# Performance work log

Hardware: AMD Instinct MI355X
Metric: run time of the kernel (lower is better)

The kernel has to match this reference:

```python
import jax, jax.numpy as jnp
import numpy as np

N_EMBD = 256
N_HEAD = 8
BATCH = 4
SEQ = 2048
NEG_BIAS = -1000000000.0


def setup_inputs() -> dict:
    key = jax.random.key(0)
    ks = jax.random.split(key, 5)
    scale = 1.0 / np.sqrt(N_EMBD)
    x = jax.random.normal(ks[0], (BATCH, SEQ, N_EMBD), dtype=jnp.float32)
    # torch Linear weight layout: (out_features, in_features)
    Wq = jax.random.normal(ks[1], (N_EMBD * N_HEAD, N_EMBD), dtype=jnp.float32) * scale
    Wk = jax.random.normal(ks[2], (N_EMBD * N_HEAD, N_EMBD), dtype=jnp.float32) * scale
    Wv = jax.random.normal(ks[3], (N_EMBD * N_HEAD, N_EMBD), dtype=jnp.float32) * scale
    Wo = jax.random.normal(ks[4], (N_EMBD, N_EMBD * N_HEAD), dtype=jnp.float32) * scale / np.sqrt(N_HEAD)
    return {"x": x, "Wq": Wq, "Wk": Wk, "Wv": Wv, "Wo": Wo}


def reference(x, Wq, Wk, Wv, Wo):
    B, L, E = x.shape
    H, D = N_HEAD, N_EMBD  # d_head == n_embd in this module
    # projections: x @ W.T, then split heads -> (B, H, L, D)
    def proj(W):
        y = jnp.einsum('ble,fe->blf', x, W)  # (B, L, H*D)
        return y.reshape(B, L, H, D).transpose(0, 2, 1, 3)
    q, k, v = proj(Wq), proj(Wk), proj(Wv)
    scores = jnp.einsum('bhld,bhmd->bhlm', q, k) * (E ** -0.5)
    # first (non-causal) softmax over full rows
    attn = jax.nn.softmax(scores, axis=-1)
    # causal mask replaces disallowed probs with large negative bias, then softmax again
    causal = jnp.tril(jnp.ones((L, L), dtype=bool))
    attn = jnp.where(causal[None, None], attn, jnp.asarray(NEG_BIAS, attn.dtype))
    attn = jax.nn.softmax(attn, axis=-1)
    out = jnp.einsum('bhlm,bhmd->bhld', attn, v)  # (B, H, L, D)
    out = out.transpose(0, 2, 1, 3).reshape(B, L, H * D)
    return jnp.einsum('blf,ef->ble', out, Wo)  # (B, L, E)
```

## Files before the change

kernel.cpp:

```cpp
#include <hip/hip_runtime.h>
#include <stdint.h>

typedef unsigned short ushort_t;
typedef __attribute__((ext_vector_type(8))) short bf16x8;
typedef __attribute__((ext_vector_type(4))) short s16x4;
typedef __attribute__((ext_vector_type(4))) float f32x4;
typedef __attribute__((ext_vector_type(4))) unsigned short us4;

#define DEV __device__ __forceinline__

DEV ushort_t f2bf(float f) {
    unsigned int u = __float_as_uint(f);
    u += 0x7fffu + ((u >> 16) & 1u);
    return (ushort_t)(u >> 16);
}

DEV void async16(const ushort_t* g, ushort_t* l) {
    __builtin_amdgcn_global_load_lds(
        (const __attribute__((address_space(1))) void*)g,
        (__attribute__((address_space(3))) void*)l,
        16, 0, 0);
}

DEV void barrier_lgkm() {
    __asm__ volatile("s_waitcnt lgkmcnt(0)\n\ts_barrier" ::: "memory");
}
DEV void barrier_vm8() {
    __asm__ volatile("s_waitcnt vmcnt(8)\n\ts_barrier" ::: "memory");
}
DEV void barrier_vm0() {
    __asm__ volatile("s_waitcnt vmcnt(0)\n\ts_barrier" ::: "memory");
}

__global__ void convert_kernel(const float* __restrict__ x, const float* __restrict__ wq,
                               const float* __restrict__ wk, const float* __restrict__ wv,
                               const float* __restrict__ wo,
                               ushort_t* __restrict__ xb, ushort_t* __restrict__ wqb,
                               ushort_t* __restrict__ wkb, ushort_t* __restrict__ wvb,
                               ushort_t* __restrict__ wob)
{
    const int i = blockIdx.x * 256 + threadIdx.x;
    const float* src; ushort_t* dst; int off;
    if (i < 524288)      { src = x;  dst = xb;  off = i; }
    else if (i < 655360) { src = wq; dst = wqb; off = i - 524288; }
    else if (i < 786432) { src = wk; dst = wkb; off = i - 655360; }
    else if (i < 917504) { src = wv; dst = wvb; off = i - 786432; }
    else                 { src = wo; dst = wob; off = i - 917504; }
    const float4 v = ((const float4*)src)[off];
    us4 o;
    o[0] = f2bf(v.x); o[1] = f2bf(v.y); o[2] = f2bf(v.z); o[3] = f2bf(v.w);
    ((us4*)dst)[off] = o;
}

__global__ __launch_bounds__(256, 2) void gemm_qkv_kernel(
    const ushort_t* __restrict__ A, const ushort_t* __restrict__ Bm,
    void* __restrict__ C0, void* __restrict__ C1, void* __restrict__ C2)
{
    __shared__ ushort_t At[128 * 64];
    __shared__ ushort_t Bt[128 * 64];

    const int tid  = threadIdx.x;
    const int wave = tid >> 6;
    const int lane = tid & 63;
    const int quad = lane >> 4;
    const int l15  = lane & 15;
    const int mhalf = wave >> 1;
    const int nhalf = wave & 1;
    const int m0 = blockIdx.x * 128;
    const int n0 = blockIdx.y * 128;
    const int K = 256;

    f32x4 acc[4][4];
#pragma unroll
    for (int mf = 0; mf < 4; ++mf)
#pragma unroll
        for (int nf = 0; nf < 4; ++nf)
#pragma unroll
            for (int r = 0; r < 4; ++r) acc[mf][nf][r] = 0.f;

    const int crow = (lane & 7) ^ (lane >> 3);

    for (int k0 = 0; k0 < K; k0 += 64) {
        __syncthreads();
#pragma unroll
        for (int t = 0; t < 4; ++t) {
            const int row = wave * 32 + t * 8 + (lane >> 3);
            async16(A + (size_t)(m0 + row) * K + k0 + crow * 8,
                    At + (wave * 32 + t * 8) * 64 + lane * 8);
            async16(Bm + (size_t)(n0 + row) * K + k0 + crow * 8,
                    Bt + (wave * 32 + t * 8) * 64 + lane * 8);
        }
        __syncthreads();
#pragma unroll
        for (int ks = 0; ks < 2; ++ks) {
            bf16x8 af[4], bf[4];
#pragma unroll
            for (int mf = 0; mf < 4; ++mf) {
                const int ml = mhalf * 64 + mf * 16 + l15;
                const int c = (ks * 4 + quad) ^ (ml & 7);
                af[mf] = *(const bf16x8*)(At + ml * 64 + c * 8);
            }
#pragma unroll
            for (int nf = 0; nf < 4; ++nf) {
                const int nl = nhalf * 64 + nf * 16 + l15;
                const int c = (ks * 4 + quad) ^ (nl & 7);
                bf[nf] = *(const bf16x8*)(Bt + nl * 64 + c * 8);
            }
#pragma unroll
            for (int mf = 0; mf < 4; ++mf)
#pragma unroll
                for (int nf = 0; nf < 4; ++nf)
                    acc[mf][nf] = __builtin_amdgcn_mfma_f32_16x16x32_bf16(
                        af[mf], bf[nf], acc[mf][nf], 0, 0, 0);
        }
    }

    const int sel = n0 >> 11;
    if (sel == 2) {
#pragma unroll
        for (int mf = 0; mf < 4; ++mf)
#pragma unroll
            for (int nf = 0; nf < 4; ++nf) {
                const int row = m0 + mhalf * 64 + mf * 16 + quad * 4;
                const int colv = (n0 - 4096) + nhalf * 64 + nf * 16 + l15;
                const int b_ = row >> 11, l_ = row & 2047;
                const int h_ = colv >> 8, d_ = colv & 255;
                us4 pk;
#pragma unroll
                for (int r = 0; r < 4; ++r) pk[r] = f2bf(acc[mf][nf][r]);
                *(us4*)((ushort_t*)C2 +
                        (((size_t)(b_ * 8 + h_) * 256 + d_) * 2048 + l_)) = pk;
            }
    } else {
        ushort_t* dst = sel ? (ushort_t*)C1 : (ushort_t*)C0;
#pragma unroll
        for (int mf = 0; mf < 4; ++mf)
#pragma unroll
            for (int nf = 0; nf < 4; ++nf)
#pragma unroll
                for (int r = 0; r < 4; ++r) {
                    const int row = m0 + mhalf * 64 + mf * 16 + quad * 4 + r;
                    const int col = (n0 & 2047) + nhalf * 64 + nf * 16 + l15;
                    dst[(size_t)row * 2048 + col] = f2bf(acc[mf][nf][r]);
                }
    }
}

__global__ __launch_bounds__(256, 4) void gemm_out_kernel(
    const ushort_t* __restrict__ A, const ushort_t* __restrict__ Bm,
    float* __restrict__ C)
{
    __shared__ ushort_t At[64 * 64];
    __shared__ ushort_t Bt[128 * 64];

    const int tid  = threadIdx.x;
    const int wave = tid >> 6;
    const int lane = tid & 63;
    const int quad = lane >> 4;
    const int l15  = lane & 15;
    const int mhalf = wave >> 1;
    const int nhalf = wave & 1;
    const int m0 = blockIdx.x * 64;
    const int n0 = blockIdx.y * 128;

    f32x4 acc[2][4];
#pragma unroll
    for (int mf = 0; mf < 2; ++mf)
#pragma unroll
        for (int nf = 0; nf < 4; ++nf)
#pragma unroll
            for (int r = 0; r < 4; ++r) acc[mf][nf][r] = 0.f;

    const int crow = (lane & 7) ^ (lane >> 3);

    for (int k0 = 0; k0 < 2048; k0 += 64) {
        __syncthreads();
#pragma unroll
        for (int t = 0; t < 2; ++t) {
            const int row = wave * 16 + t * 8 + (lane >> 3);
            async16(A + (size_t)(m0 + row) * 2048 + k0 + crow * 8,
                    At + (wave * 16 + t * 8) * 64 + lane * 8);
        }
#pragma unroll
        for (int t = 0; t < 4; ++t) {
            const int row = wave * 32 + t * 8 + (lane >> 3);
            async16(Bm + (size_t)(n0 + row) * 2048 + k0 + crow * 8,
                    Bt + (wave * 32 + t * 8) * 64 + lane * 8);
        }
        __syncthreads();
#pragma unroll
        for (int ks = 0; ks < 2; ++ks) {
            bf16x8 af[2], bf[4];
#pragma unroll
            for (int mf = 0; mf < 2; ++mf) {
                const int ml = mhalf * 32 + mf * 16 + l15;
                const int c = (ks * 4 + quad) ^ (ml & 7);
                af[mf] = *(const bf16x8*)(At + ml * 64 + c * 8);
            }
#pragma unroll
            for (int nf = 0; nf < 4; ++nf) {
                const int nl = nhalf * 64 + nf * 16 + l15;
                const int c = (ks * 4 + quad) ^ (nl & 7);
                bf[nf] = *(const bf16x8*)(Bt + nl * 64 + c * 8);
            }
#pragma unroll
            for (int mf = 0; mf < 2; ++mf)
#pragma unroll
                for (int nf = 0; nf < 4; ++nf)
                    acc[mf][nf] = __builtin_amdgcn_mfma_f32_16x16x32_bf16(
                        af[mf], bf[nf], acc[mf][nf], 0, 0, 0);
        }
    }

#pragma unroll
    for (int mf = 0; mf < 2; ++mf)
#pragma unroll
        for (int nf = 0; nf < 4; ++nf)
#pragma unroll
            for (int r = 0; r < 4; ++r) {
                const int row = m0 + mhalf * 32 + mf * 16 + quad * 4 + r;
                const int col = n0 + nhalf * 64 + nf * 16 + l15;
                C[(size_t)row * 256 + col] = acc[mf][nf][r];
            }
}

__global__ __launch_bounds__(256, 4) void pass1_kernel(
    const ushort_t* __restrict__ q_ws, const ushort_t* __restrict__ k_ws,
    float* __restrict__ rz_ws)
{
    __shared__ ushort_t Kt[64 * 256];
    __shared__ float zred[2][64];

    const float SCALE = 0.0625f;
    const int tid  = threadIdx.x;
    const int wave = tid >> 6;
    const int lane = tid & 63;
    const int quad = lane >> 4;
    const int l15  = lane & 15;
    const int ihalf = wave >> 1;
    const int jhalf = wave & 1;

    const int g  = blockIdx.x;
    const int bh = ((g >> 8) << 3) | (g & 7);
    const int it = (g >> 3) & 31;
    const int b = bh >> 3, h = bh & 7;
    const int i0 = it * 64;

    const size_t qkbase = (size_t)b * 2048 * 2048 + (size_t)h * 256;

    bf16x8 qf[2][8];
#pragma unroll
    for (int ng = 0; ng < 2; ++ng) {
        const int i_l = ihalf * 32 + ng * 16 + l15;
        const ushort_t* qr = q_ws + qkbase + (size_t)(i0 + i_l) * 2048;
#pragma unroll
        for (int ks = 0; ks < 8; ++ks)
            qf[ng][ks] = *(const bf16x8*)(qr + ks * 32 + quad * 8);
    }

    float z[2] = {0.f, 0.f};

    for (int jt = 0; jt < 32; ++jt) {
        const int j0 = jt * 64;
        __syncthreads();
        {
            const ushort_t* kb = k_ws + qkbase + (size_t)j0 * 2048;
#pragma unroll
            for (int t = 0; t < 8; ++t) {
                const int row = wave * 16 + t * 2 + (lane >> 5);
                const int c = (lane & 31) ^ (row & 7);
                async16(kb + (size_t)row * 2048 + c * 8,
                        Kt + (wave * 16 + t * 2) * 256 + lane * 8);
            }
        }
        __syncthreads();

        f32x4 sacc[2][2];
#pragma unroll
        for (int a = 0; a < 2; ++a)
#pragma unroll
            for (int c = 0; c < 2; ++c)
#pragma unroll
                for (int r = 0; r < 4; ++r) sacc[a][c][r] = 0.f;

#pragma unroll
        for (int ks = 0; ks < 8; ++ks) {
            bf16x8 af[2];
#pragma unroll
            for (int mg = 0; mg < 2; ++mg) {
                const int j_l = jhalf * 32 + mg * 16 + l15;
                const int c = (ks * 4 + quad) ^ (j_l & 7);
                af[mg] = *(const bf16x8*)(Kt + j_l * 256 + c * 8);
            }
#pragma unroll
            for (int mg = 0; mg < 2; ++mg)
#pragma unroll
                for (int ng = 0; ng < 2; ++ng)
                    sacc[mg][ng] = __builtin_amdgcn_mfma_f32_16x16x32_bf16(
                        af[mg], qf[ng][ks], sacc[mg][ng], 0, 0, 0);
        }

#pragma unroll
        for (int ng = 0; ng < 2; ++ng)
#pragma unroll
            for (int mg = 0; mg < 2; ++mg)
#pragma unroll
                for (int r = 0; r < 4; ++r)
                    z[ng] += __expf(sacc[mg][ng][r] * SCALE);
    }

#pragma unroll
    for (int ng = 0; ng < 2; ++ng) {
        z[ng] += __shfl_xor(z[ng], 16);
        z[ng] += __shfl_xor(z[ng], 32);
    }
    __syncthreads();
    if (quad == 0) {
#pragma unroll
        for (int ng = 0; ng < 2; ++ng) {
            const int i_l = ihalf * 32 + ng * 16 + l15;
            zred[jhalf][i_l] = z[ng];
        }
    }
    __syncthreads();
    if (tid < 64)
        rz_ws[(size_t)bh * 2048 + i0 + tid] = 1.0f / (zred[0][tid] + zred[1][tid]);
}

__global__ __launch_bounds__(256, 1) void pass2_kernel(
    const ushort_t* __restrict__ q_ws, const ushort_t* __restrict__ k_ws,
    const ushort_t* __restrict__ vt_ws, const float* __restrict__ rz_ws,
    ushort_t* __restrict__ attn_out)
{
    __shared__ ushort_t Kb[2][32 * 256];
    __shared__ ushort_t Vb[2][256 * 32];
    __shared__ ushort_t Wt[64 * 32];
    __shared__ float dred[128];

    const float SCALE = 0.0625f;
    const int tid  = threadIdx.x;
    const int wave = tid >> 6;
    const int lane = tid & 63;
    const int quad = lane >> 4;
    const int l15  = lane & 15;
    const int ihalf = wave >> 1;
    const int jhalf = wave & 1;

    const int g  = blockIdx.x;
    const int bh = ((g >> 8) << 3) | (g & 7);
    const int it = 31 - ((g >> 3) & 31);
    const int b = bh >> 3, h = bh & 7;
    const int i0 = it * 64;
    const int jtmax = 2 * it + 1;

    const size_t qkbase = (size_t)b * 2048 * 2048 + (size_t)h * 256;
    const size_t vtbase = (size_t)bh * 256 * 2048;

    bf16x8 qf[2][8];
#pragma unroll
    for (int ng = 0; ng < 2; ++ng) {
        const int i_l = ihalf * 32 + ng * 16 + l15;
        const ushort_t* qr = q_ws + qkbase + (size_t)(i0 + i_l) * 2048;
#pragma unroll
        for (int ks = 0; ks < 8; ++ks)
            qf[ng][ks] = *(const bf16x8*)(qr + ks * 32 + quad * 8);
    }
    float rzrow[2];
#pragma unroll
    for (int ng = 0; ng < 2; ++ng)
        rzrow[ng] = rz_ws[(size_t)bh * 2048 + i0 + ihalf * 32 + ng * 16 + l15];

    f32x4 oacc[2][8];
#pragma unroll
    for (int mg = 0; mg < 2; ++mg)
#pragma unroll
        for (int nf = 0; nf < 8; ++nf)
#pragma unroll
            for (int r = 0; r < 4; ++r) oacc[mg][nf][r] = 0.f;
    float den[2] = {0.f, 0.f};

    const int krow_ = wave * 8 + (lane >> 5);
    const int vrow_ = wave * 64 + (lane >> 2);
#define STAGE_TILE(jt_, pb_)                                                  \
    {                                                                         \
        const ushort_t* kb_ = k_ws + qkbase + (size_t)(jt_) * 32 * 2048;      \
        const ushort_t* vb_ = vt_ws + vtbase + (size_t)(jt_) * 32;            \
        _Pragma("unroll")                                                     \
        for (int t = 0; t < 4; ++t) {                                         \
            const int kr = krow_ + t * 2;                                     \
            const int kc = (lane & 31) ^ (kr & 7);                            \
            async16(kb_ + (size_t)kr * 2048 + kc * 8,                         \
                    Kb[pb_] + (wave * 8 + t * 2) * 256 + lane * 8);           \
        }                                                                     \
        _Pragma("unroll")                                                     \
        for (int t = 0; t < 4; ++t) {                                         \
            const int vr = vrow_ + t * 16;                                    \
            const int vc = (lane & 3) ^ ((vr ^ (vr >> 2)) & 3);               \
            async16(vb_ + (size_t)vr * 2048 + vc * 8,                         \
                    Vb[pb_] + (wave * 64 + t * 16) * 32 + lane * 8);          \
        }                                                                     \
    }

    STAGE_TILE(0, 0);

    const int iblo = it * 4 + ihalf * 2;

    for (int jt = 0; jt <= jtmax; ++jt) {
        const int p = jt & 1;
        barrier_lgkm();
        if (jt < jtmax) {
            STAGE_TILE(jt + 1, 1 - p);
            barrier_vm8();
        } else {
            barrier_vm0();
        }

        const int jb16 = jt * 2 + jhalf;
        if (jb16 <= iblo + 1) {
            f32x4 sacc[2];
#pragma unroll
            for (int ng = 0; ng < 2; ++ng)
#pragma unroll
                for (int r = 0; r < 4; ++r) sacc[ng][r] = 0.f;
#pragma unroll
            for (int ks = 0; ks < 8; ++ks) {
                const int j_l = jhalf * 16 + l15;
                const int c = (ks * 4 + quad) ^ (j_l & 7);
                const bf16x8 af = *(const bf16x8*)(Kb[p] + j_l * 256 + c * 8);
#pragma unroll
                for (int ng = 0; ng < 2; ++ng)
                    sacc[ng] = __builtin_amdgcn_mfma_f32_16x16x32_bf16(
                        af, qf[ng][ks], sacc[ng], 0, 0, 0);
            }
            const bool need_mask = (jb16 >= iblo);
#pragma unroll
            for (int ng = 0; ng < 2; ++ng) {
                const int di = (i0 + ihalf * 32 + ng * 16 + l15)
                             - (jt * 32 + jhalf * 16 + quad * 4);
                us4 wp;
#pragma unroll
                for (int r = 0; r < 4; ++r) {
                    const float pr = __expf(sacc[ng][r] * SCALE) * rzrow[ng];
                    float w = __expf(pr);
                    if (need_mask && (r > di)) w = 0.f;
                    den[ng] += w;
                    wp[r] = f2bf(w);
                }
                const int row = ihalf * 32 + ng * 16 + l15;
                const int c = (jhalf * 4 + quad) ^ (l15 & 7);
                *(us4*)(Wt + row * 32 + c * 4) = wp;
            }
        } else {
            const us4 zz = {0, 0, 0, 0};
#pragma unroll
            for (int ng = 0; ng < 2; ++ng) {
                const int row = ihalf * 32 + ng * 16 + l15;
                const int c = (jhalf * 4 + quad) ^ (l15 & 7);
                *(us4*)(Wt + row * 32 + c * 4) = zz;
            }
        }
        barrier_lgkm();

        if (jt <= it * 2 + ihalf) {
            bf16x8 aw[2];
#pragma unroll
            for (int mg = 0; mg < 2; ++mg) {
                const int row = ihalf * 32 + mg * 16 + l15;
                const s16x4 lo = *(const s16x4*)(Wt + row * 32 + ((2 * quad)     ^ (l15 & 7)) * 4);
                const s16x4 hi = *(const s16x4*)(Wt + row * 32 + ((2 * quad + 1) ^ (l15 & 7)) * 4);
                union { s16x4 hh[2]; bf16x8 v; } u;
                u.hh[0] = lo; u.hh[1] = hi;
                aw[mg] = u.v;
            }
#pragma unroll
            for (int nf = 0; nf < 8; ++nf) {
                const int d = jhalf * 128 + nf * 16 + l15;
                const int c = quad ^ ((d ^ (d >> 2)) & 3);
                const bf16x8 bv = *(const bf16x8*)(Vb[p] + d * 32 + c * 8);
                oacc[0][nf] = __builtin_amdgcn_mfma_f32_16x16x32_bf16(aw[0], bv, oacc[0][nf], 0, 0, 0);
                oacc[1][nf] = __builtin_amdgcn_mfma_f32_16x16x32_bf16(aw[1], bv, oacc[1][nf], 0, 0, 0);
            }
        }
    }
#undef STAGE_TILE

#pragma unroll
    for (int ng = 0; ng < 2; ++ng) {
        den[ng] += __shfl_xor(den[ng], 16);
        den[ng] += __shfl_xor(den[ng], 32);
    }
    __syncthreads();
    if (quad == 0) {
#pragma unroll
        for (int ng = 0; ng < 2; ++ng)
            dred[(ihalf * 2 + jhalf) * 32 + ng * 16 + l15] = den[ng];
    }
    __syncthreads();
#pragma unroll
    for (int mg = 0; mg < 2; ++mg) {
#pragma unroll
        for (int r = 0; r < 4; ++r) {
            const int il = mg * 16 + quad * 4 + r;
            const float dt = dred[(ihalf * 2) * 32 + il] + dred[(ihalf * 2 + 1) * 32 + il];
            const float rd = 1.0f / dt;
            ushort_t* orow = attn_out + qkbase + (size_t)(i0 + ihalf * 32 + il) * 2048;
#pragma unroll
            for (int nf = 0; nf < 8; ++nf)
                orow[jhalf * 128 + nf * 16 + l15] = f2bf(oacc[mg][nf][r] * rd);
        }
    }
}

extern "C" void kernel_launch(void* const* d_in, const int* in_sizes, int n_in,
                              void* d_out, int out_size, void* d_ws, size_t ws_size,
                              hipStream_t stream) {
    const float* x  = (const float*)d_in[0];
    const float* Wq = (const float*)d_in[1];
    const float* Wk = (const float*)d_in[2];
    const float* Wv = (const float*)d_in[3];
    const float* Wo = (const float*)d_in[4];

    char* ws = (char*)d_ws;
    ushort_t* xb    = (ushort_t*)(ws);
    ushort_t* wqb   = (ushort_t*)(ws + 4194304);
    ushort_t* wkb   = (ushort_t*)(ws + 5242880);
    ushort_t* wvb   = (ushort_t*)(ws + 6291456);
    ushort_t* wob   = (ushort_t*)(ws + 7340032);
    ushort_t* q_ws  = (ushort_t*)(ws + 8388608);
    ushort_t* k_ws  = (ushort_t*)(ws + 41943040);
    ushort_t* vt_ws = (ushort_t*)(ws + 75497472);
    ushort_t* ao_ws = (ushort_t*)(ws + 109051904);
    float*    rz_ws = (float*)   (ws + 142606336);

    convert_kernel<<<4096, 256, 0, stream>>>(x, Wq, Wk, Wv, Wo, xb, wqb, wkb, wvb, wob);

    gemm_qkv_kernel<<<dim3(64, 48), 256, 0, stream>>>(xb, wqb, q_ws, k_ws, vt_ws);

    pass1_kernel<<<1024, 256, 0, stream>>>(q_ws, k_ws, rz_ws);
    pass2_kernel<<<1024, 256, 0, stream>>>(q_ws, k_ws, vt_ws, rz_ws, ao_ws);

    gemm_out_kernel<<<dim3(128, 2), 256, 0, stream>>>(ao_ws, wob, (float*)d_out);
}
```

Measured before the change: 375.5 us.

## Double-buffer K in pass1 and read V fragments directly from global in pass2

Pass1 now uses two 32-row K buffers in LDS and prefetches the next tile asynchronously while computing the current one, which removes one barrier per iteration. Pass2 drops the V staging buffer in LDS and loads the V^T MFMA fragments per lane straight from global memory into registers. It also raises launch bounds to two blocks per CU, using the freed LDS for higher occupancy. The trade-off is strided, less coalesced global reads for V, which rely on the cache, plus more register pressure from holding eight V fragments per wave.

After: 437.6 us. 16.5% more time.

```diff
diff --git a/kernel.cpp b/kernel.cpp
--- a/kernel.cpp
+++ b/kernel.cpp
@@ -24,12 +24,6 @@
 
 DEV void barrier_lgkm() {
     __asm__ volatile("s_waitcnt lgkmcnt(0)\n\ts_barrier" ::: "memory");
-}
-DEV void barrier_vm8() {
-    __asm__ volatile("s_waitcnt vmcnt(8)\n\ts_barrier" ::: "memory");
-}
-DEV void barrier_vm0() {
-    __asm__ volatile("s_waitcnt vmcnt(0)\n\ts_barrier" ::: "memory");
 }
 
 __global__ void convert_kernel(const float* __restrict__ x, const float* __restrict__ wq,
@@ -228,7 +222,7 @@
     const ushort_t* __restrict__ q_ws, const ushort_t* __restrict__ k_ws,
     float* __restrict__ rz_ws)
 {
-    __shared__ ushort_t Kt[64 * 256];
+    __shared__ ushort_t Kb[2][32 * 256];
     __shared__ float zred[2][64];
 
     const float SCALE = 0.0625f;
@@ -248,6 +242,21 @@
 
     const size_t qkbase = (size_t)b * 2048 * 2048 + (size_t)h * 256;
 
+    const int krow_ = wave * 8 + (lane >> 5);
+#define STAGE_K1(jt_, pb_)                                                    \
+    {                                                                         \
+        const ushort_t* kb_ = k_ws + qkbase + (size_t)(jt_) * 32 * 2048;      \
+        _Pragma("unroll")                                                     \
+        for (int t = 0; t < 4; ++t) {                                         \
+            const int kr = krow_ + t * 2;                                     \
+            const int kc = (lane & 31) ^ (kr & 7);                            \
+            async16(kb_ + (size_t)kr * 2048 + kc * 8,                         \
+                    Kb[pb_] + (wave * 8 + t * 2) * 256 + lane * 8);           \
+        }                                                                     \
+    }
+
+    STAGE_K1(0, 0);
+
     bf16x8 qf[2][8];
 #pragma unroll
     for (int ng = 0; ng < 2; ++ng) {
@@ -260,54 +269,34 @@
 
     float z[2] = {0.f, 0.f};
 
-    for (int jt = 0; jt < 32; ++jt) {
-        const int j0 = jt * 64;
+    for (int jt = 0; jt < 64; ++jt) {
+        const int p = jt & 1;
         __syncthreads();
-        {
-            const ushort_t* kb = k_ws + qkbase + (size_t)j0 * 2048;
-#pragma unroll
-            for (int t = 0; t < 8; ++t) {
-                const int row = wave * 16 + t * 2 + (lane >> 5);
-                const int c = (lane & 31) ^ (row & 7);
-                async16(kb + (size_t)row * 2048 + c * 8,
-                        Kt + (wave * 16 + t * 2) * 256 + lane * 8);
-            }
-        }
-        __syncthreads();
-
-        f32x4 sacc[2][2];
-#pragma unroll
-        for (int a = 0; a < 2; ++a)
-#pragma unroll
-            for (int c = 0; c < 2; ++c)
-#pragma unroll
-                for (int r = 0; r < 4; ++r) sacc[a][c][r] = 0.f;
+        if (jt < 63) STAGE_K1(jt + 1, 1 - p);
+
+        f32x4 sacc[2];
+#pragma unroll
+        for (int ng = 0; ng < 2; ++ng)
+#pragma unroll
+            for (int r = 0; r < 4; ++r) sacc[ng][r] = 0.f;
 
 #pragma unroll
         for (int ks = 0; ks < 8; ++ks) {
-            bf16x8 af[2];
-#pragma unroll
-            for (int mg = 0; mg < 2; ++mg) {
-                const int j_l = jhalf * 32 + mg * 16 + l15;
-                const int c = (ks * 4 + quad) ^ (j_l & 7);
-                af[mg] = *(const bf16x8*)(Kt + j_l * 256 + c * 8);
-            }
-#pragma unroll
-            for (int mg = 0; mg < 2; ++mg)
-#pragma unroll
-                for (int ng = 0; ng < 2; ++ng)
-                    sacc[mg][ng] = __builtin_amdgcn_mfma_f32_16x16x32_bf16(
-                        af[mg], qf[ng][ks], sacc[mg][ng], 0, 0, 0);
-        }
-
+            const int j_l = jhalf * 16 + l15;
+            const int c = (ks * 4 + quad) ^ (j_l & 7);
+            const bf16x8 af = *(const bf16x8*)(Kb[p] + j_l * 256 + c * 8);
+#pragma unroll
+            for (int ng = 0; ng < 2; ++ng)
+                sacc[ng] = __builtin_amdgcn_mfma_f32_16x16x32_bf16(
+                    af, qf[ng][ks], sacc[ng], 0, 0, 0);
+        }
 #pragma unroll
         for (int ng = 0; ng < 2; ++ng)
 #pragma unroll
-            for (int mg = 0; mg < 2; ++mg)
-#pragma unroll
-                for (int r = 0; r < 4; ++r)
-                    z[ng] += __expf(sacc[mg][ng][r] * SCALE);
-    }
+            for (int r = 0; r < 4; ++r)
+                z[ng] += __expf(sacc[ng][r] * SCALE);
+    }
+#undef STAGE_K1
 
 #pragma unroll
     for (int ng = 0; ng < 2; ++ng) {
@@ -317,23 +306,20 @@
     __syncthreads();
     if (quad == 0) {
 #pragma unroll
-        for (int ng = 0; ng < 2; ++ng) {
-            const int i_l = ihalf * 32 + ng * 16 + l15;
-            zred[jhalf][i_l] = z[ng];
-        }
+        for (int ng = 0; ng < 2; ++ng)
+            zred[jhalf][ihalf * 32 + ng * 16 + l15] = z[ng];
     }
     __syncthreads();
     if (tid < 64)
         rz_ws[(size_t)bh * 2048 + i0 + tid] = 1.0f / (zred[0][tid] + zred[1][tid]);
 }
 
-__global__ __launch_bounds__(256, 1) void pass2_kernel(
+__global__ __launch_bounds__(256, 2) void pass2_kernel(
     const ushort_t* __restrict__ q_ws, const ushort_t* __restrict__ k_ws,
     const ushort_t* __restrict__ vt_ws, const float* __restrict__ rz_ws,
     ushort_t* __restrict__ attn_out)
 {
     __shared__ ushort_t Kb[2][32 * 256];
-    __shared__ ushort_t Vb[2][256 * 32];
     __shared__ ushort_t Wt[64 * 32];
     __shared__ float dred[128];
 
@@ -356,35 +342,10 @@
     const size_t qkbase = (size_t)b * 2048 * 2048 + (size_t)h * 256;
     const size_t vtbase = (size_t)bh * 256 * 2048;
 
-    bf16x8 qf[2][8];
-#pragma unroll
-    for (int ng = 0; ng < 2; ++ng) {
-        const int i_l = ihalf * 32 + ng * 16 + l15;
-        const ushort_t* qr = q_ws + qkbase + (size_t)(i0 + i_l) * 2048;
-#pragma unroll
-        for (int ks = 0; ks < 8; ++ks)
-            qf[ng][ks] = *(const bf16x8*)(qr + ks * 32 + quad * 8);
-    }
-    float rzrow[2];
-#pragma unroll
-    for (int ng = 0; ng < 2; ++ng)
-        rzrow[ng] = rz_ws[(size_t)bh * 2048 + i0 + ihalf * 32 + ng * 16 + l15];
-
-    f32x4 oacc[2][8];
-#pragma unroll
-    for (int mg = 0; mg < 2; ++mg)
-#pragma unroll
-        for (int nf = 0; nf < 8; ++nf)
-#pragma unroll
-            for (int r = 0; r < 4; ++r) oacc[mg][nf][r] = 0.f;
-    float den[2] = {0.f, 0.f};
-
     const int krow_ = wave * 8 + (lane >> 5);
-    const int vrow_ = wave * 64 + (lane >> 2);
-#define STAGE_TILE(jt_, pb_)                                                  \
+#define STAGE_K2(jt_, pb_)                                                    \
     {                                                                         \
         const ushort_t* kb_ = k_ws + qkbase + (size_t)(jt_) * 32 * 2048;      \
-        const ushort_t* vb_ = vt_ws + vtbase + (size_t)(jt_) * 32;            \
         _Pragma("unroll")                                                     \
         for (int t = 0; t < 4; ++t) {                                         \
             const int kr = krow_ + t * 2;                                     \
@@ -392,27 +353,49 @@
             async16(kb_ + (size_t)kr * 2048 + kc * 8,                         \
                     Kb[pb_] + (wave * 8 + t * 2) * 256 + lane * 8);           \
         }                                                                     \
-        _Pragma("unroll")                                                     \
-        for (int t = 0; t < 4; ++t) {                                         \
-            const int vr = vrow_ + t * 16;                                    \
-            const int vc = (lane & 3) ^ ((vr ^ (vr >> 2)) & 3);               \
-            async16(vb_ + (size_t)vr * 2048 + vc * 8,                         \
-                    Vb[pb_] + (wave * 64 + t * 16) * 32 + lane * 8);          \
-        }                                                                     \
-    }
-
-    STAGE_TILE(0, 0);
+    }
+
+    STAGE_K2(0, 0);
+
+    bf16x8 qf[2][8];
+#pragma unroll
+    for (int ng = 0; ng < 2; ++ng) {
+        const int i_l = ihalf * 32 + ng * 16 + l15;
+        const ushort_t* qr = q_ws + qkbase + (size_t)(i0 + i_l) * 2048;
+#pragma unroll
+        for (int ks = 0; ks < 8; ++ks)
+            qf[ng][ks] = *(const bf16x8*)(qr + ks * 32 + quad * 8);
+    }
+    float rzrow[2];
+#pragma unroll
+    for (int ng = 0; ng < 2; ++ng)
+        rzrow[ng] = rz_ws[(size_t)bh * 2048 + i0 + ihalf * 32 + ng * 16 + l15];
+
+    const ushort_t* vfrag = vt_ws + vtbase +
+        (size_t)(jhalf * 128 + l15) * 2048 + quad * 8;
+
+    f32x4 oacc[2][8];
+#pragma unroll
+    for (int mg = 0; mg < 2; ++mg)
+#pragma unroll
+        for (int nf = 0; nf < 8; ++nf)
+#pragma unroll
+            for (int r = 0; r < 4; ++r) oacc[mg][nf][r] = 0.f;
+    float den[2] = {0.f, 0.f};
 
     const int iblo = it * 4 + ihalf * 2;
 
     for (int jt = 0; jt <= jtmax; ++jt) {
         const int p = jt & 1;
-        barrier_lgkm();
-        if (jt < jtmax) {
-            STAGE_TILE(jt + 1, 1 - p);
-            barrier_vm8();
-        } else {
-            barrier_vm0();
+        __syncthreads();
+        if (jt < jtmax) STAGE_K2(jt + 1, 1 - p);
+
+        bf16x8 bv[8];
+        {
+            const ushort_t* vb = vfrag + jt * 32;
+#pragma unroll
+            for (int nf = 0; nf < 8; ++nf)
+                bv[nf] = *(const bf16x8*)(vb + (size_t)(nf * 16) * 2048);
         }
 
         const int jb16 = jt * 2 + jhalf;
@@ -474,15 +457,12 @@
             }
 #pragma unroll
             for (int nf = 0; nf < 8; ++nf) {
-                const int d = jhalf * 128 + nf * 16 + l15;
-                const int c = quad ^ ((d ^ (d >> 2)) & 3);
-                const bf16x8 bv = *(const bf16x8*)(Vb[p] + d * 32 + c * 8);
-                oacc[0][nf] = __builtin_amdgcn_mfma_f32_16x16x32_bf16(aw[0], bv, oacc[0][nf], 0, 0, 0);
-                oacc[1][nf] = __builtin_amdgcn_mfma_f32_16x16x32_bf16(aw[1], bv, oacc[1][nf], 0, 0, 0);
-            }
-        }
-    }
-#undef STAGE_TILE
+                oacc[0][nf] = __builtin_amdgcn_mfma_f32_16x16x32_bf16(aw[0], bv[nf], oacc[0][nf], 0, 0, 0);
+                oacc[1][nf] = __builtin_amdgcn_mfma_f32_16x16x32_bf16(aw[1], bv[nf], oacc[1][nf], 0, 0, 0);
+            }
+        }
+    }
+#undef STAGE_K2
 
 #pragma unroll
     for (int ng = 0; ng < 2; ++ng) {
```
